# Kernel optimization log

Measured on AMD Instinct MI355X. Metric: run time of the kernel, lower is better.

Reference implementation:

```python
import jax, jax.numpy as jnp
import numpy as np

N, L, D, H = 2, 2048, 1024, 16
Dh = D // H          # 64
HIST = 2048          # history_len
SCALE = D ** 0.5     # note: module scales by sqrt(model_dim), not sqrt(head_dim)


def setup_inputs() -> dict:
    key = jax.random.key(0)
    ks = jax.random.split(key, 10)
    f = lambda k, s, sc=1.0: jax.random.normal(k, s, dtype=jnp.float32) * sc
    i = jnp.arange(L)
    causal = i[None, :] > i[:, None]            # mask future
    old = i[None, :] <= i[:, None] - HIST       # mask beyond history window
    mask = causal | old                          # True = masked, (L, L)
    return {
        "values": f(ks[0], (N, L, D)),
        "keys": f(ks[1], (N, L, D)),
        "query": f(ks[2], (N, L, D)),
        "origin_values": f(ks[3], (N, L, D)),
        "origin_keys": f(ks[4], (N, L, D)),
        "Wv": f(ks[5], (Dh, Dh), 0.1),
        "Wk": f(ks[6], (Dh, Dh), 0.1),
        "Wq": f(ks[7], (Dh, Dh), 0.1),
        "fc_w": f(ks[8], (D, D), 0.03),
        "fc_b": jnp.zeros((D,), dtype=jnp.float32),
        "mask": mask,
    }


def reference(values, keys, query, origin_values, origin_keys, Wv, Wk, Wq, fc_w, fc_b, mask):
    # forward(..., ref_sample=True): mfpca_attention path.
    # origin_keys/values are projected exactly as the prior ref_sample=False call stored them.
    split = lambda x: x.reshape(N, L, H, Dh)
    v = split(values) @ Wv.T        # (N, L, H, Dh)  torch Linear: x @ W^T, no bias
    k = split(keys) @ Wk.T
    q = split(query) @ Wq.T
    ov = split(origin_values) @ Wv.T
    ok = split(origin_keys) @ Wk.T

    energy = jnp.einsum('nqhd,nkhd->nhqk', q, ok)       # (N, H, L, L)
    samp_energy = jnp.einsum('nlhd,nlhd->nhl', q, k)    # (N, H, L)
    eye = jnp.eye(L, dtype=bool)
    # energy.diagonal().copy_(samp_energy)
    energy = jnp.where(eye, samp_energy[:, :, None, :], energy)
    energy = jnp.where(mask, jnp.float32(-1e20), energy)
    scores = jax.nn.softmax(energy / SCALE, axis=-1)
    diag_scores = jnp.diagonal(scores, axis1=2, axis2=3)    # (N, H, L)
    scores_nodiag = jnp.where(eye, 0.0, scores)
    # NOTE: original einsum output is indexed by l (not q) -- reproduced faithfully.
    origin_attention = jnp.einsum('nhql,nlhd->nlhd', scores_nodiag, ov)
    samp_attention = jnp.einsum('nhl,nlhd->nlhd', diag_scores, v)
    attention = (samp_attention + origin_attention).reshape(N, L, D)
    return attention @ fc_w.T + fc_b
```

## Files before the change

kernel.cpp:

```cpp
#include <hip/hip_runtime.h>

#define NB 2
#define LL 2048
#define DD 1024
#define HH 16
#define NHH (NB*HH)
#define LT (LL/64)
#define KT16 (LL/16)
#define CEXP 0.0450842200277801f

typedef __bf16 bf16x8 __attribute__((ext_vector_type(8)));
typedef unsigned short u16x8 __attribute__((ext_vector_type(8)));
typedef float f32x4 __attribute__((ext_vector_type(4)));

#define MFMA16 __builtin_amdgcn_mfma_f32_16x16x32_bf16
#define EXP2 __builtin_amdgcn_exp2f

__device__ __forceinline__ unsigned short f2bf(float f) {
    unsigned u = __float_as_uint(f);
    return (unsigned short)((u + 0x7fffu + ((u >> 16) & 1u)) >> 16);
}
__device__ __forceinline__ float bf2f(unsigned short u) {
    return __uint_as_float(((unsigned)u) << 16);
}
__device__ __forceinline__ bf16x8 ldfrag(const unsigned short* p) {
    return *reinterpret_cast<const bf16x8*>(p);
}
__device__ __forceinline__ bf16x8 cvt8v(float4 a, float4 b) {
    u16x8 u;
    u[0]=f2bf(a.x); u[1]=f2bf(a.y); u[2]=f2bf(a.z); u[3]=f2bf(a.w);
    u[4]=f2bf(b.x); u[5]=f2bf(b.y); u[6]=f2bf(b.z); u[7]=f2bf(b.w);
    return __builtin_bit_cast(bf16x8, u);
}
__device__ __forceinline__ ushort4 pack4(f32x4 d, float sc) {
    ushort4 o;
    o.x = f2bf(d[0]*sc); o.y = f2bf(d[1]*sc); o.z = f2bf(d[2]*sc); o.w = f2bf(d[3]*sc);
    return o;
}
__device__ __forceinline__ void gload16(const unsigned short* g, unsigned short* l) {
    __builtin_amdgcn_global_load_lds(
        (const __attribute__((address_space(1))) unsigned int*)g,
        (__attribute__((address_space(3))) unsigned int*)l, 16, 0, 0);
}

__global__ __launch_bounds__(256) void prep_kernel(
    const float* __restrict__ Wk, const float* __restrict__ Wq,
    const float* __restrict__ Wv, unsigned short* __restrict__ wfrag,
    const float* __restrict__ fc_w, unsigned short* __restrict__ fcwb,
    float* __restrict__ zreg)
{
    const int bid = blockIdx.x;
    const int t = threadIdx.x;
    if (bid < 6) {
        const int s = bid * 256 + t;
        const int m = s >> 9;
        const int rem = s & 511;
        const int f = rem >> 6;
        const int lane = rem & 63;
        const int n16 = lane & 15, quad = lane >> 4;
        const int mt = f >> 1, half = f & 1;
        const float* W = (m == 0) ? Wk : (m == 1) ? Wq : Wv;
        const float* p = W + (mt*16 + n16)*64 + quad*8 + half*32;
        float4 a = *reinterpret_cast<const float4*>(p);
        float4 b = *reinterpret_cast<const float4*>(p + 4);
        *reinterpret_cast<bf16x8*>(wfrag + (size_t)s * 8) = cvt8v(a, b);
    } else if (bid < 6 + 1024) {
        const int idx = (bid - 6) * 1024 + t * 4;
        float4 wv = *reinterpret_cast<const float4*>(fc_w + idx);
        ushort4 o;
        o.x = f2bf(wv.x); o.y = f2bf(wv.y); o.z = f2bf(wv.z); o.w = f2bf(wv.w);
        *reinterpret_cast<ushort4*>(fcwb + idx) = o;
    } else {
        const int i = (bid - 1030) * 1024 + t * 4;
        *reinterpret_cast<float4*>(zreg + i) = (float4){0.f, 0.f, 0.f, 0.f};
    }
}

__global__ __launch_bounds__(256) void proj_kernel(
    const float* __restrict__ values, const float* __restrict__ keys,
    const float* __restrict__ query,  const float* __restrict__ ovals,
    const float* __restrict__ okeys,  const unsigned short* __restrict__ wfrag,
    unsigned short* __restrict__ qb, unsigned short* __restrict__ okb,
    unsigned short* __restrict__ vb, unsigned short* __restrict__ ovb,
    float* __restrict__ ediag)
{
    const int t = threadIdx.x;
    const int w = t >> 6;
    const int lane = t & 63;
    const int n16 = lane & 15;
    const int quad = lane >> 4;
    const int h = blockIdx.y;
    const int row = blockIdx.x * 64 + w * 16 + n16;
    const int nn = row >> 11;
    const int ll = row & 2047;
    const size_t xoff  = (size_t)row * DD + h * 64 + quad * 8;
    const size_t qbase = (((size_t)(nn * HH + h)) * LL + ll) * 64;
    const size_t vbase = (size_t)row * DD + h * 64;

    if (blockIdx.z == 0) {
        const float4* kp = reinterpret_cast<const float4*>(keys  + xoff);
        const float4* qp = reinterpret_cast<const float4*>(query + xoff);
        const float4* op = reinterpret_cast<const float4*>(okeys + xoff);
        float4 k0 = kp[0], k1 = kp[1], k2 = kp[8], k3 = kp[9];
        float4 q0 = qp[0], q1 = qp[1], q2 = qp[8], q3 = qp[9];
        float4 o0 = op[0], o1 = op[1], o2 = op[8], o3 = op[9];
        bf16x8 wk[8], wq[8];
#pragma unroll
        for (int f = 0; f < 8; ++f) {
            wk[f] = ldfrag(wfrag + (size_t)(f * 64 + lane) * 8);
            wq[f] = ldfrag(wfrag + (size_t)((8 + f) * 64 + lane) * 8);
        }
        bf16x8 xk0 = cvt8v(k0, k1), xk1 = cvt8v(k2, k3);
        bf16x8 xq0 = cvt8v(q0, q1), xq1 = cvt8v(q2, q3);
        bf16x8 xo0 = cvt8v(o0, o1), xo1 = cvt8v(o2, o3);
        f32x4 ka[4], qa[4];
#pragma unroll
        for (int mt = 0; mt < 4; ++mt) {
            f32x4 d = {0.f,0.f,0.f,0.f};
            d = MFMA16(wk[mt*2], xk0, d, 0,0,0);
            ka[mt] = MFMA16(wk[mt*2+1], xk1, d, 0,0,0);
        }
#pragma unroll
        for (int mt = 0; mt < 4; ++mt) {
            f32x4 d = {0.f,0.f,0.f,0.f};
            d = MFMA16(wq[mt*2], xq0, d, 0,0,0);
            qa[mt] = MFMA16(wq[mt*2+1], xq1, d, 0,0,0);
            *reinterpret_cast<ushort4*>(qb + qbase + mt*16 + quad*4) = pack4(qa[mt], CEXP);
        }
#pragma unroll
        for (int mt = 0; mt < 4; ++mt) {
            f32x4 d = {0.f,0.f,0.f,0.f};
            d = MFMA16(wk[mt*2], xo0, d, 0,0,0);
            d = MFMA16(wk[mt*2+1], xo1, d, 0,0,0);
            *reinterpret_cast<ushort4*>(okb + qbase + mt*16 + quad*4) = pack4(d, 1.0f);
        }
        float p = 0.f;
#pragma unroll
        for (int mt = 0; mt < 4; ++mt)
            p += qa[mt][0]*ka[mt][0] + qa[mt][1]*ka[mt][1]
               + qa[mt][2]*ka[mt][2] + qa[mt][3]*ka[mt][3];
        p += __shfl_xor(p, 16);
        p += __shfl_xor(p, 32);
        if (lane < 16)
            ediag[((size_t)(nn * HH + h)) * LL + ll] = p;
    } else {
        const float4* vp = reinterpret_cast<const float4*>(values + xoff);
        const float4* op = reinterpret_cast<const float4*>(ovals  + xoff);
        float4 v0 = vp[0], v1 = vp[1], v2 = vp[8], v3 = vp[9];
        float4 o0 = op[0], o1 = op[1], o2 = op[8], o3 = op[9];
        bf16x8 wv[8];
#pragma unroll
        for (int f = 0; f < 8; ++f)
            wv[f] = ldfrag(wfrag + (size_t)((16 + f) * 64 + lane) * 8);
        bf16x8 xv0 = cvt8v(v0, v1), xv1 = cvt8v(v2, v3);
        bf16x8 xo0 = cvt8v(o0, o1), xo1 = cvt8v(o2, o3);
#pragma unroll
        for (int mt = 0; mt < 4; ++mt) {
            f32x4 d = {0.f,0.f,0.f,0.f};
            d = MFMA16(wv[mt*2], xv0, d, 0,0,0);
            d = MFMA16(wv[mt*2+1], xv1, d, 0,0,0);
            *reinterpret_cast<ushort4*>(vb + vbase + mt*16 + quad*4) = pack4(d, 1.0f);
        }
#pragma unroll
        for (int mt = 0; mt < 4; ++mt) {
            f32x4 d = {0.f,0.f,0.f,0.f};
            d = MFMA16(wv[mt*2], xo0, d, 0,0,0);
            d = MFMA16(wv[mt*2+1], xo1, d, 0,0,0);
            *reinterpret_cast<ushort4*>(ovb + vbase + mt*16 + quad*4) = pack4(d, 1.0f);
        }
    }
}

__global__ __launch_bounds__(256) void zrow_part(
    const unsigned short* __restrict__ qb, const unsigned short* __restrict__ okb,
    float* __restrict__ Zbuf)
{
    const int bid = blockIdx.x;
    const int xcd = bid & 7;
    const int slot = bid >> 3;
    const int nh = xcd * 4 + (slot >> 5);
    const int px = slot & 31;
    const int pair = px >> 1;
    const int s = px & 1;
    const int t = threadIdx.x;
    const int w = t >> 6;
    const int lane = t & 63;
    const int n = lane & 15;
    const int quad = lane >> 4;
    const size_t base = (size_t)nh * (LL * 64);
    const size_t nhL = (size_t)nh * LL;
    const int r0 = 4 * s + w;

#pragma unroll
    for (int half = 0; half < 2; ++half) {
        const int qt = half ? (31 - pair) : pair;
        const int kend = 4 * qt + 4;

        bf16x8 bq[4][2];
#pragma unroll
        for (int ct = 0; ct < 4; ++ct) {
            const unsigned short* p = qb + base + (size_t)(qt*64 + ct*16 + n) * 64 + quad * 8;
            bq[ct][0] = ldfrag(p); bq[ct][1] = ldfrag(p + 32);
        }

        float zacc[4] = {0.f, 0.f, 0.f, 0.f};

        bf16x8 a0A = {}, a1A = {}, a0B = {}, a1B = {}, a0C = {}, a1C = {};
        if (r0 < kend) {
            const unsigned short* p = okb + base + (size_t)(r0*16 + n) * 64 + quad * 8;
            a0A = ldfrag(p); a1A = ldfrag(p + 32);
        }
        if (r0 + 8 < kend) {
            const unsigned short* p = okb + base + (size_t)((r0+8)*16 + n) * 64 + quad * 8;
            a0B = ldfrag(p); a1B = ldfrag(p + 32);
        }
        if (r0 + 16 < kend) {
            const unsigned short* p = okb + base + (size_t)((r0+16)*16 + n) * 64 + quad * 8;
            a0C = ldfrag(p); a1C = ldfrag(p + 32);
        }
        for (int kt = r0; kt < kend; kt += 8) {
            bf16x8 a0 = a0A, a1 = a1A;
            a0A = a0B; a1A = a1B; a0B = a0C; a1B = a1C;
            if (kt + 24 < kend) {
                const unsigned short* p = okb + base + (size_t)((kt+24)*16 + n) * 64 + quad * 8;
                a0C = ldfrag(p); a1C = ldfrag(p + 32);
            }
            const int dk = kt - 4*qt;
#pragma unroll
            for (int ct = 0; ct < 4; ++ct) {
                if (ct < dk) continue;
                f32x4 d = {0.f,0.f,0.f,0.f};
                d = MFMA16(a0, bq[ct][0], d, 0,0,0);
                d = MFMA16(a1, bq[ct][1], d, 0,0,0);
                if (ct == dk) {
#pragma unroll
                    for (int r = 0; r < 4; ++r)
                        if (quad*4 + r < n) zacc[ct] += EXP2(d[r]);
                } else {
#pragma unroll
                    for (int r = 0; r < 4; ++r) zacc[ct] += EXP2(d[r]);
                }
            }
        }

#pragma unroll
        for (int ct = 0; ct < 4; ++ct) {
            float z = zacc[ct];
            z += __shfl_down(z, 32);
            z += __shfl_down(z, 16);
            if (lane < 16)
                atomicAdd(&Zbuf[nhL + qt*64 + ct*16 + lane], z);
        }
    }
}

__global__ __launch_bounds__(256) void colsum_part(
    const unsigned short* __restrict__ qb, const unsigned short* __restrict__ okb,
    const float* __restrict__ Zbuf, const float* __restrict__ ediag,
    float* __restrict__ colsum)
{
    const int bid = blockIdx.x;
    const int xcd = bid & 7;
    const int slot = bid >> 3;
    const int nh = xcd * 4 + (slot >> 5);
    const int px = slot & 31;
    const int pair = px >> 1;
    const int s = px & 1;
    const int t = threadIdx.x;
    const int w = t >> 6;
    const int lane = t & 63;
    const int n = lane & 15;
    const int quad = lane >> 4;
    const size_t base = (size_t)nh * (LL * 64);
    const size_t nhL = (size_t)nh * LL;
    const int r0 = 4 * s + w;

#pragma unroll
    for (int half = 0; half < 2; ++half) {
        const int lt = half ? (31 - pair) : pair;

        bf16x8 bl[4][2];
#pragma unroll
        for (int ct = 0; ct < 4; ++ct) {
            const unsigned short* p = okb + base + (size_t)(lt*64 + ct*16 + n) * 64 + quad * 8;
            bl[ct][0] = ldfrag(p); bl[ct][1] = ldfrag(p + 32);
        }

        float cacc[4] = {0.f, 0.f, 0.f, 0.f};

        const int kstart = 4*lt + r0;
        bf16x8 a0A = {}, a1A = {}, a0B = {}, a1B = {}, a0C = {}, a1C = {};
        float4 zA = {0,0,0,0}, zB = {0,0,0,0}, zC = {0,0,0,0};
        float4 eA = {0,0,0,0}, eB = {0,0,0,0}, eC = {0,0,0,0};
        if (kstart < KT16) {
            const unsigned short* p = qb + base + (size_t)(kstart*16 + n) * 64 + quad * 8;
            a0A = ldfrag(p); a1A = ldfrag(p + 32);
            zA = *reinterpret_cast<const float4*>(Zbuf  + nhL + kstart*16 + quad*4);
            eA = *reinterpret_cast<const float4*>(ediag + nhL + kstart*16 + quad*4);
        }
        if (kstart + 8 < KT16) {
            const unsigned short* p = qb + base + (size_t)((kstart+8)*16 + n) * 64 + quad * 8;
            a0B = ldfrag(p); a1B = ldfrag(p + 32);
            zB = *reinterpret_cast<const float4*>(Zbuf  + nhL + (kstart+8)*16 + quad*4);
            eB = *reinterpret_cast<const float4*>(ediag + nhL + (kstart+8)*16 + quad*4);
        }
        if (kstart + 16 < KT16) {
            const unsigned short* p = qb + base + (size_t)((kstart+16)*16 + n) * 64 + quad * 8;
            a0C = ldfrag(p); a1C = ldfrag(p + 32);
            zC = *reinterpret_cast<const float4*>(Zbuf  + nhL + (kstart+16)*16 + quad*4);
            eC = *reinterpret_cast<const float4*>(ediag + nhL + (kstart+16)*16 + quad*4);
        }
        for (int kt = kstart; kt < KT16; kt += 8) {
            bf16x8 a0 = a0A, a1 = a1A; const float4 zv = zA, ev = eA;
            a0A = a0B; a1A = a1B; zA = zB; eA = eB;
            a0B = a0C; a1B = a1C; zB = zC; eB = eC;
            if (kt + 24 < KT16) {
                const unsigned short* p = qb + base + (size_t)((kt+24)*16 + n) * 64 + quad * 8;
                a0C = ldfrag(p); a1C = ldfrag(p + 32);
                zC = *reinterpret_cast<const float4*>(Zbuf  + nhL + (kt+24)*16 + quad*4);
                eC = *reinterpret_cast<const float4*>(ediag + nhL + (kt+24)*16 + quad*4);
            }
            float4 izv;
            izv.x = 1.f / (zv.x + EXP2(ev.x * CEXP));
            izv.y = 1.f / (zv.y + EXP2(ev.y * CEXP));
            izv.z = 1.f / (zv.z + EXP2(ev.z * CEXP));
            izv.w = 1.f / (zv.w + EXP2(ev.w * CEXP));
            const int dk = kt - 4*lt;
#pragma unroll
            for (int ct = 0; ct < 4; ++ct) {
                if (ct > dk) continue;
                f32x4 d = {0.f,0.f,0.f,0.f};
                d = MFMA16(a0, bl[ct][0], d, 0,0,0);
                d = MFMA16(a1, bl[ct][1], d, 0,0,0);
                if (ct == dk) {
                    if (quad*4 + 0 > n) cacc[ct] += EXP2(d[0]) * izv.x;
                    if (quad*4 + 1 > n) cacc[ct] += EXP2(d[1]) * izv.y;
                    if (quad*4 + 2 > n) cacc[ct] += EXP2(d[2]) * izv.z;
                    if (quad*4 + 3 > n) cacc[ct] += EXP2(d[3]) * izv.w;
                } else {
                    cacc[ct] += EXP2(d[0]) * izv.x;
                    cacc[ct] += EXP2(d[1]) * izv.y;
                    cacc[ct] += EXP2(d[2]) * izv.z;
                    cacc[ct] += EXP2(d[3]) * izv.w;
                }
            }
        }

#pragma unroll
        for (int ct = 0; ct < 4; ++ct) {
            float c = cacc[ct];
            c += __shfl_down(c, 32);
            c += __shfl_down(c, 16);
            if (lane < 16)
                atomicAdd(&colsum[nhL + lt*64 + ct*16 + lane], c);
        }
    }
}

#define LOADA(vS, ovS, zS, eS, csS, k) do {                                \
    vS  = ldfrag(pv  + (k)*32);                                            \
    ovS = ldfrag(pov + (k)*32);                                            \
    zS  = Zbuf  [scbase + ((k)>>1)*LL];                                    \
    eS  = ediag [scbase + ((k)>>1)*LL];                                    \
    csS = colsum[scbase + ((k)>>1)*LL];                                    \
} while (0)

#define CVTWRITE(vS, ovS, zS, eS, csS, dst) do {                           \
    const float de_ = EXP2(eS * CEXP);                                     \
    const float ds_ = de_ * (1.f / (zS + de_));                            \
    u16x8 vu_ = __builtin_bit_cast(u16x8, vS);                             \
    u16x8 ou_ = __builtin_bit_cast(u16x8, ovS);                            \
    u16x8 o_;                                                              \
    _Pragma("unroll")                                                      \
    for (int i_ = 0; i_ < 8; ++i_)                                         \
        o_[i_] = f2bf(ds_ * bf2f(vu_[i_]) + csS * bf2f(ou_[i_]));          \
    *reinterpret_cast<u16x8*>(dst) = o_;                                   \
} while (0)

#define COMPUTE(Abuf, Bbuf) do {                                           \
    bf16x8 af_[4], bf_[2];                                                 \
    _Pragma("unroll")                                                      \
    for (int mt = 0; mt < 4; ++mt)                                         \
        af_[mt] = ldfrag((Abuf) + (wr*64 + mt*16 + n)*32 + quad*8);        \
    _Pragma("unroll")                                                      \
    for (int nt = 0; nt < 2; ++nt)                                         \
        bf_[nt] = ldfrag((Bbuf) + (wc*32 + nt*16 + n)*32 + quad*8);        \
    _Pragma("unroll")                                                      \
    for (int mt = 0; mt < 4; ++mt)                                         \
        _Pragma("unroll")                                                  \
        for (int nt = 0; nt < 2; ++nt)                                     \
            acc[mt][nt] = MFMA16(af_[mt], bf_[nt], acc[mt][nt], 0,0,0);    \
} while (0)

__global__ __launch_bounds__(512) void out_kernel(
    const unsigned short* __restrict__ vb, const unsigned short* __restrict__ ovb,
    const float* __restrict__ Zbuf, const float* __restrict__ ediag,
    const float* __restrict__ colsum,
    const unsigned short* __restrict__ fcwb, const float* __restrict__ fc_b,
    float* __restrict__ out)
{
    __shared__ unsigned short lds[2][2][128 * 32];

    const int bid = blockIdx.x;
    const int swz = (bid & 7) * 32 + (bid >> 3);
    const int ct = swz & 7;
    const int rt = swz >> 3;
    const int row0 = rt * 128, col0 = ct * 128;

    const int t = threadIdx.x;
    const int w = t >> 6, lane = t & 63;
    const int n = lane & 15, quad = lane >> 4;
    const int wr = w >> 2, wc = w & 3;

    const int arow = row0 + (t >> 2);
    const unsigned short* pv  = vb  + (size_t)arow * DD + (t & 3) * 8;
    const unsigned short* pov = ovb + (size_t)arow * DD + (t & 3) * 8;
    const int scbase = (arow >> 11) * (HH * LL) + (arow & 2047);
    const unsigned short* gb = fcwb + (size_t)(col0 + (t >> 2)) * DD + (t & 3) * 8;
    unsigned short* la0 = &lds[0][0][t * 8];
    unsigned short* lb0 = &lds[0][1][t * 8];
    unsigned short* la1 = &lds[1][0][t * 8];
    unsigned short* lb1 = &lds[1][1][t * 8];
    const unsigned short* A0 = &lds[0][0][0];
    const unsigned short* B0 = &lds[0][1][0];
    const unsigned short* A1 = &lds[1][0][0];
    const unsigned short* B1 = &lds[1][1][0];

    f32x4 acc[4][2];
#pragma unroll
    for (int mt = 0; mt < 4; ++mt)
#pragma unroll
        for (int nt = 0; nt < 2; ++nt) acc[mt][nt] = (f32x4){0.f, 0.f, 0.f, 0.f};

    bf16x8 vP, ovP, vQ, ovQ; float zP, eP, csP, zQ, eQ, csQ;
    LOADA(vP, ovP, zP, eP, csP, 0);
    LOADA(vQ, ovQ, zQ, eQ, csQ, 1);
    gload16(gb, lb0);
    CVTWRITE(vP, ovP, zP, eP, csP, la0);
    __syncthreads();

    for (int kt = 0; kt < 32; kt += 2) {
        gload16(gb + (kt + 1) * 32, lb1);
        if (kt + 2 < 32) LOADA(vP, ovP, zP, eP, csP, kt + 2);
        COMPUTE(A0, B0);
        CVTWRITE(vQ, ovQ, zQ, eQ, csQ, la1);
        __syncthreads();
        if (kt + 2 < 32) {
            gload16(gb + (kt + 2) * 32, lb0);
            if (kt + 3 < 32) LOADA(vQ, ovQ, zQ, eQ, csQ, kt + 3);
        }
        COMPUTE(A1, B1);
        if (kt + 2 < 32) CVTWRITE(vP, ovP, zP, eP, csP, la0);
        __syncthreads();
    }

#pragma unroll
    for (int nt = 0; nt < 2; ++nt) {
        const int col = col0 + wc * 32 + nt * 16 + n;
        const float bias = fc_b[col];
#pragma unroll
        for (int mt = 0; mt < 4; ++mt)
#pragma unroll
            for (int r = 0; r < 4; ++r)
                out[(size_t)(row0 + wr * 64 + mt * 16 + quad * 4 + r) * DD + col]
                    = acc[mt][nt][r] + bias;
    }
}

extern "C" void kernel_launch(void* const* d_in, const int* in_sizes, int n_in,
                              void* d_out, int out_size, void* d_ws, size_t ws_size,
                              hipStream_t stream) {
    const float* values = (const float*)d_in[0];
    const float* keys   = (const float*)d_in[1];
    const float* query  = (const float*)d_in[2];
    const float* ovals  = (const float*)d_in[3];
    const float* okeys  = (const float*)d_in[4];
    const float* Wv     = (const float*)d_in[5];
    const float* Wk     = (const float*)d_in[6];
    const float* Wq     = (const float*)d_in[7];
    const float* fc_w   = (const float*)d_in[8];
    const float* fc_b   = (const float*)d_in[9];
    float* out = (float*)d_out;

    float* ws      = (float*)d_ws;
    float* ediag   = ws;
    float* Zbuf    = ediag + 65536;
    float* colsum  = Zbuf + 65536;
    unsigned short* qb   = (unsigned short*)(colsum + 65536);
    unsigned short* okb  = qb   + 4194304;
    unsigned short* vb   = okb  + 4194304;
    unsigned short* ovb  = vb   + 4194304;
    unsigned short* fcwb = ovb  + 4194304;
    unsigned short* wfrag = fcwb + 1048576;

    prep_kernel<<<dim3(1158), 256, 0, stream>>>(Wk, Wq, Wv, wfrag, fc_w, fcwb, Zbuf);
    proj_kernel<<<dim3(64, 16, 2), 256, 0, stream>>>(
        values, keys, query, ovals, okeys, wfrag, qb, okb, vb, ovb, ediag);
    zrow_part<<<dim3(1024), 256, 0, stream>>>(qb, okb, Zbuf);
    colsum_part<<<dim3(1024), 256, 0, stream>>>(qb, okb, Zbuf, ediag, colsum);
    out_kernel<<<dim3(256), 512, 0, stream>>>(vb, ovb, Zbuf, ediag, colsum, fcwb, fc_b, out);
}
```

Baseline: 247.3 us.

## Stage key/query strips in double-buffered LDS and drop atomics in row/column sums

zrow_part and colsum_part now give each block one 64-row tile of one head. The block streams the opposite operand in 64-row strips through a double-buffered, XOR-swizzled LDS buffer filled with global_load_lds, and the four waves share each strip. Before, every wave loaded MFMA fragments straight from global memory. Because each output tile is now owned by a single block, results are stored directly instead of through atomicAdd, which removes the zero-init of Zbuf/colsum from prep_kernel. The cost is a barrier per strip and the loss of the earlier pairing of short and long tiles. Work per block is now uneven, though blocks with the most work are issued first.

Result: faster. 222.6 us (-10.0%).

```diff
diff --git a/kernel.cpp b/kernel.cpp
--- a/kernel.cpp
+++ b/kernel.cpp
@@ -46,8 +46,7 @@
 __global__ __launch_bounds__(256) void prep_kernel(
     const float* __restrict__ Wk, const float* __restrict__ Wq,
     const float* __restrict__ Wv, unsigned short* __restrict__ wfrag,
-    const float* __restrict__ fc_w, unsigned short* __restrict__ fcwb,
-    float* __restrict__ zreg)
+    const float* __restrict__ fc_w, unsigned short* __restrict__ fcwb)
 {
     const int bid = blockIdx.x;
     const int t = threadIdx.x;
@@ -64,15 +63,12 @@
         float4 a = *reinterpret_cast<const float4*>(p);
         float4 b = *reinterpret_cast<const float4*>(p + 4);
         *reinterpret_cast<bf16x8*>(wfrag + (size_t)s * 8) = cvt8v(a, b);
-    } else if (bid < 6 + 1024) {
+    } else {
         const int idx = (bid - 6) * 1024 + t * 4;
         float4 wv = *reinterpret_cast<const float4*>(fc_w + idx);
         ushort4 o;
         o.x = f2bf(wv.x); o.y = f2bf(wv.y); o.z = f2bf(wv.z); o.w = f2bf(wv.w);
         *reinterpret_cast<ushort4*>(fcwb + idx) = o;
-    } else {
-        const int i = (bid - 1030) * 1024 + t * 4;
-        *reinterpret_cast<float4*>(zreg + i) = (float4){0.f, 0.f, 0.f, 0.f};
     }
 }
 
@@ -175,13 +171,11 @@
     const unsigned short* __restrict__ qb, const unsigned short* __restrict__ okb,
     float* __restrict__ Zbuf)
 {
+    __shared__ unsigned short slds[2][64 * 64];
+
     const int bid = blockIdx.x;
-    const int xcd = bid & 7;
-    const int slot = bid >> 3;
-    const int nh = xcd * 4 + (slot >> 5);
-    const int px = slot & 31;
-    const int pair = px >> 1;
-    const int s = px & 1;
+    const int nh = bid & 31;
+    const int qt = 31 - (bid >> 5);
     const int t = threadIdx.x;
     const int w = t >> 6;
     const int lane = t & 63;
@@ -189,69 +183,62 @@
     const int quad = lane >> 4;
     const size_t base = (size_t)nh * (LL * 64);
     const size_t nhL = (size_t)nh * LL;
-    const int r0 = 4 * s + w;
-
-#pragma unroll
-    for (int half = 0; half < 2; ++half) {
-        const int qt = half ? (31 - pair) : pair;
-        const int kend = 4 * qt + 4;
-
-        bf16x8 bq[4][2];
-#pragma unroll
-        for (int ct = 0; ct < 4; ++ct) {
-            const unsigned short* p = qb + base + (size_t)(qt*64 + ct*16 + n) * 64 + quad * 8;
-            bq[ct][0] = ldfrag(p); bq[ct][1] = ldfrag(p + 32);
-        }
-
-        float zacc[4] = {0.f, 0.f, 0.f, 0.f};
-
-        bf16x8 a0A = {}, a1A = {}, a0B = {}, a1B = {}, a0C = {}, a1C = {};
-        if (r0 < kend) {
-            const unsigned short* p = okb + base + (size_t)(r0*16 + n) * 64 + quad * 8;
-            a0A = ldfrag(p); a1A = ldfrag(p + 32);
-        }
-        if (r0 + 8 < kend) {
-            const unsigned short* p = okb + base + (size_t)((r0+8)*16 + n) * 64 + quad * 8;
-            a0B = ldfrag(p); a1B = ldfrag(p + 32);
-        }
-        if (r0 + 16 < kend) {
-            const unsigned short* p = okb + base + (size_t)((r0+16)*16 + n) * 64 + quad * 8;
-            a0C = ldfrag(p); a1C = ldfrag(p + 32);
-        }
-        for (int kt = r0; kt < kend; kt += 8) {
-            bf16x8 a0 = a0A, a1 = a1A;
-            a0A = a0B; a1A = a1B; a0B = a0C; a1B = a1C;
-            if (kt + 24 < kend) {
-                const unsigned short* p = okb + base + (size_t)((kt+24)*16 + n) * 64 + quad * 8;
-                a0C = ldfrag(p); a1C = ldfrag(p + 32);
+
+    const unsigned short* bp = qb + base + (size_t)(qt*64 + w*16 + n) * 64 + quad * 8;
+    const bf16x8 bq0 = ldfrag(bp);
+    const bf16x8 bq1 = ldfrag(bp + 32);
+
+    const int srow = t >> 3;
+    const int schunk = (t & 7) ^ (srow & 7);
+    const int soff = srow * 64 + schunk * 8;
+    const int nst = qt + 1;
+
+    {
+        const unsigned short* s0 = okb + base + soff;
+        gload16(s0, &slds[0][t * 8]);
+        gload16(s0 + 32 * 64, &slds[0][2048 + t * 8]);
+    }
+    __syncthreads();
+
+    const int rs0 = (quad ^ (n & 7)) * 8;
+    const int rs1 = ((quad + 4) ^ (n & 7)) * 8;
+
+    float zacc = 0.f;
+    int buf = 0;
+    for (int si = 0; si < nst; ++si) {
+        if (si + 1 < nst) {
+            const unsigned short* s0 = okb + base + (size_t)((si + 1) * 64) * 64 + soff;
+            gload16(s0, &slds[buf ^ 1][t * 8]);
+            gload16(s0 + 32 * 64, &slds[buf ^ 1][2048 + t * 8]);
+        }
+        const unsigned short* S = &slds[buf][0];
+        const bool dstrip = (si == qt);
+#pragma unroll
+        for (int sub = 0; sub < 4; ++sub) {
+            if (dstrip && sub > w) continue;
+            const int row = sub * 16 + n;
+            const bf16x8 a0 = ldfrag(S + row * 64 + rs0);
+            const bf16x8 a1 = ldfrag(S + row * 64 + rs1);
+            f32x4 d = {0.f, 0.f, 0.f, 0.f};
+            d = MFMA16(a0, bq0, d, 0, 0, 0);
+            d = MFMA16(a1, bq1, d, 0, 0, 0);
+            if (dstrip && sub == w) {
+#pragma unroll
+                for (int r = 0; r < 4; ++r)
+                    if (quad * 4 + r < n) zacc += EXP2(d[r]);
+            } else {
+#pragma unroll
+                for (int r = 0; r < 4; ++r) zacc += EXP2(d[r]);
             }
-            const int dk = kt - 4*qt;
-#pragma unroll
-            for (int ct = 0; ct < 4; ++ct) {
-                if (ct < dk) continue;
-                f32x4 d = {0.f,0.f,0.f,0.f};
-                d = MFMA16(a0, bq[ct][0], d, 0,0,0);
-                d = MFMA16(a1, bq[ct][1], d, 0,0,0);
-                if (ct == dk) {
-#pragma unroll
-                    for (int r = 0; r < 4; ++r)
-                        if (quad*4 + r < n) zacc[ct] += EXP2(d[r]);
-                } else {
-#pragma unroll
-                    for (int r = 0; r < 4; ++r) zacc[ct] += EXP2(d[r]);
-                }
-            }
-        }
-
-#pragma unroll
-        for (int ct = 0; ct < 4; ++ct) {
-            float z = zacc[ct];
-            z += __shfl_down(z, 32);
-            z += __shfl_down(z, 16);
-            if (lane < 16)
-                atomicAdd(&Zbuf[nhL + qt*64 + ct*16 + lane], z);
-        }
-    }
+        }
+        __syncthreads();
+        buf ^= 1;
+    }
+
+    zacc += __shfl_down(zacc, 32);
+    zacc += __shfl_down(zacc, 16);
+    if (lane < 16)
+        Zbuf[nhL + qt * 64 + w * 16 + lane] = zacc;
 }
 
 __global__ __launch_bounds__(256) void colsum_part(
@@ -259,13 +246,12 @@
     const float* __restrict__ Zbuf, const float* __restrict__ ediag,
     float* __restrict__ colsum)
 {
+    __shared__ unsigned short slds[2][64 * 64];
+    __shared__ __align__(16) float izlds[2][64];
+
     const int bid = blockIdx.x;
-    const int xcd = bid & 7;
-    const int slot = bid >> 3;
-    const int nh = xcd * 4 + (slot >> 5);
-    const int px = slot & 31;
-    const int pair = px >> 1;
-    const int s = px & 1;
+    const int nh = bid & 31;
+    const int lt = bid >> 5;
     const int t = threadIdx.x;
     const int w = t >> 6;
     const int lane = t & 63;
@@ -273,88 +259,75 @@
     const int quad = lane >> 4;
     const size_t base = (size_t)nh * (LL * 64);
     const size_t nhL = (size_t)nh * LL;
-    const int r0 = 4 * s + w;
-
-#pragma unroll
-    for (int half = 0; half < 2; ++half) {
-        const int lt = half ? (31 - pair) : pair;
-
-        bf16x8 bl[4][2];
-#pragma unroll
-        for (int ct = 0; ct < 4; ++ct) {
-            const unsigned short* p = okb + base + (size_t)(lt*64 + ct*16 + n) * 64 + quad * 8;
-            bl[ct][0] = ldfrag(p); bl[ct][1] = ldfrag(p + 32);
-        }
-
-        float cacc[4] = {0.f, 0.f, 0.f, 0.f};
-
-        const int kstart = 4*lt + r0;
-        bf16x8 a0A = {}, a1A = {}, a0B = {}, a1B = {}, a0C = {}, a1C = {};
-        float4 zA = {0,0,0,0}, zB = {0,0,0,0}, zC = {0,0,0,0};
-        float4 eA = {0,0,0,0}, eB = {0,0,0,0}, eC = {0,0,0,0};
-        if (kstart < KT16) {
-            const unsigned short* p = qb + base + (size_t)(kstart*16 + n) * 64 + quad * 8;
-            a0A = ldfrag(p); a1A = ldfrag(p + 32);
-            zA = *reinterpret_cast<const float4*>(Zbuf  + nhL + kstart*16 + quad*4);
-            eA = *reinterpret_cast<const float4*>(ediag + nhL + kstart*16 + quad*4);
-        }
-        if (kstart + 8 < KT16) {
-            const unsigned short* p = qb + base + (size_t)((kstart+8)*16 + n) * 64 + quad * 8;
-            a0B = ldfrag(p); a1B = ldfrag(p + 32);
-            zB = *reinterpret_cast<const float4*>(Zbuf  + nhL + (kstart+8)*16 + quad*4);
-            eB = *reinterpret_cast<const float4*>(ediag + nhL + (kstart+8)*16 + quad*4);
-        }
-        if (kstart + 16 < KT16) {
-            const unsigned short* p = qb + base + (size_t)((kstart+16)*16 + n) * 64 + quad * 8;
-            a0C = ldfrag(p); a1C = ldfrag(p + 32);
-            zC = *reinterpret_cast<const float4*>(Zbuf  + nhL + (kstart+16)*16 + quad*4);
-            eC = *reinterpret_cast<const float4*>(ediag + nhL + (kstart+16)*16 + quad*4);
-        }
-        for (int kt = kstart; kt < KT16; kt += 8) {
-            bf16x8 a0 = a0A, a1 = a1A; const float4 zv = zA, ev = eA;
-            a0A = a0B; a1A = a1B; zA = zB; eA = eB;
-            a0B = a0C; a1B = a1C; zB = zC; eB = eC;
-            if (kt + 24 < KT16) {
-                const unsigned short* p = qb + base + (size_t)((kt+24)*16 + n) * 64 + quad * 8;
-                a0C = ldfrag(p); a1C = ldfrag(p + 32);
-                zC = *reinterpret_cast<const float4*>(Zbuf  + nhL + (kt+24)*16 + quad*4);
-                eC = *reinterpret_cast<const float4*>(ediag + nhL + (kt+24)*16 + quad*4);
+
+    const unsigned short* bp = okb + base + (size_t)(lt*64 + w*16 + n) * 64 + quad * 8;
+    const bf16x8 bl0 = ldfrag(bp);
+    const bf16x8 bl1 = ldfrag(bp + 32);
+
+    const int srow = t >> 3;
+    const int schunk = (t & 7) ^ (srow & 7);
+    const int soff = srow * 64 + schunk * 8;
+    const int nst = 32 - lt;
+    const int q00 = lt * 64;
+
+    {
+        const unsigned short* s0 = qb + base + (size_t)q00 * 64 + soff;
+        gload16(s0, &slds[0][t * 8]);
+        gload16(s0 + 32 * 64, &slds[0][2048 + t * 8]);
+        if (t < 64) {
+            const float z = Zbuf[nhL + q00 + t];
+            const float e = ediag[nhL + q00 + t];
+            izlds[0][t] = 1.f / (z + EXP2(e * CEXP));
+        }
+    }
+    __syncthreads();
+
+    const int rs0 = (quad ^ (n & 7)) * 8;
+    const int rs1 = ((quad + 4) ^ (n & 7)) * 8;
+
+    float cacc = 0.f;
+    int buf = 0;
+    for (int si = 0; si < nst; ++si) {
+        if (si + 1 < nst) {
+            const int qn = q00 + (si + 1) * 64;
+            const unsigned short* s0 = qb + base + (size_t)qn * 64 + soff;
+            gload16(s0, &slds[buf ^ 1][t * 8]);
+            gload16(s0 + 32 * 64, &slds[buf ^ 1][2048 + t * 8]);
+            if (t < 64) {
+                const float z = Zbuf[nhL + qn + t];
+                const float e = ediag[nhL + qn + t];
+                izlds[buf ^ 1][t] = 1.f / (z + EXP2(e * CEXP));
             }
-            float4 izv;
-            izv.x = 1.f / (zv.x + EXP2(ev.x * CEXP));
-            izv.y = 1.f / (zv.y + EXP2(ev.y * CEXP));
-            izv.z = 1.f / (zv.z + EXP2(ev.z * CEXP));
-            izv.w = 1.f / (zv.w + EXP2(ev.w * CEXP));
-            const int dk = kt - 4*lt;
-#pragma unroll
-            for (int ct = 0; ct < 4; ++ct) {
-                if (ct > dk) continue;
-                f32x4 d = {0.f,0.f,0.f,0.f};
-                d = MFMA16(a0, bl[ct][0], d, 0,0,0);
-                d = MFMA16(a1, bl[ct][1], d, 0,0,0);
-                if (ct == dk) {
-                    if (quad*4 + 0 > n) cacc[ct] += EXP2(d[0]) * izv.x;
-                    if (quad*4 + 1 > n) cacc[ct] += EXP2(d[1]) * izv.y;
-                    if (quad*4 + 2 > n) cacc[ct] += EXP2(d[2]) * izv.z;
-                    if (quad*4 + 3 > n) cacc[ct] += EXP2(d[3]) * izv.w;
-                } else {
-                    cacc[ct] += EXP2(d[0]) * izv.x;
-                    cacc[ct] += EXP2(d[1]) * izv.y;
-                    cacc[ct] += EXP2(d[2]) * izv.z;
-                    cacc[ct] += EXP2(d[3]) * izv.w;
-                }
+        }
+        const unsigned short* S = &slds[buf][0];
+        const bool dstrip = (si == 0);
+#pragma unroll
+        for (int sub = 0; sub < 4; ++sub) {
+            if (dstrip && sub < w) continue;
+            const int row = sub * 16 + n;
+            const bf16x8 a0 = ldfrag(S + row * 64 + rs0);
+            const bf16x8 a1 = ldfrag(S + row * 64 + rs1);
+            const f32x4 izv = *reinterpret_cast<const f32x4*>(&izlds[buf][sub * 16 + quad * 4]);
+            f32x4 d = {0.f, 0.f, 0.f, 0.f};
+            d = MFMA16(a0, bl0, d, 0, 0, 0);
+            d = MFMA16(a1, bl1, d, 0, 0, 0);
+            if (dstrip && sub == w) {
+#pragma unroll
+                for (int r = 0; r < 4; ++r)
+                    if (quad * 4 + r > n) cacc += EXP2(d[r]) * izv[r];
+            } else {
+#pragma unroll
+                for (int r = 0; r < 4; ++r) cacc += EXP2(d[r]) * izv[r];
             }
         }
-
-#pragma unroll
-        for (int ct = 0; ct < 4; ++ct) {
-            float c = cacc[ct];
-            c += __shfl_down(c, 32);
-            c += __shfl_down(c, 16);
-            if (lane < 16)
-                atomicAdd(&colsum[nhL + lt*64 + ct*16 + lane], c);
-        }
-    }
+        __syncthreads();
+        buf ^= 1;
+    }
+
+    cacc += __shfl_down(cacc, 32);
+    cacc += __shfl_down(cacc, 16);
+    if (lane < 16)
+        colsum[nhL + lt * 64 + w * 16 + lane] = cacc;
 }
 
 #define LOADA(vS, ovS, zS, eS, csS, k) do {                                \
@@ -493,7 +466,7 @@
     unsigned short* fcwb = ovb  + 4194304;
     unsigned short* wfrag = fcwb + 1048576;
 
-    prep_kernel<<<dim3(1158), 256, 0, stream>>>(Wk, Wq, Wv, wfrag, fc_w, fcwb, Zbuf);
+    prep_kernel<<<dim3(1030), 256, 0, stream>>>(Wk, Wq, Wv, wfrag, fc_w, fcwb);
     proj_kernel<<<dim3(64, 16, 2), 256, 0, stream>>>(
         values, keys, query, ovals, okeys, wfrag, qb, okb, vb, ovb, ediag);
     zrow_part<<<dim3(1024), 256, 0, stream>>>(qb, okb, Zbuf);
```
